# Performance work log

Hardware: AMD Instinct MI355X
Metric: run time of the kernel (lower is better)

## Reference

```python
import jax, jax.numpy as jnp
import numpy as np

DIM = 768
NUM_HEADS = 12
HEAD_DIM = DIM // NUM_HEADS
B, QLEN, KVLEN = 8, 512, 4096


def setup_inputs() -> dict:
    key = jax.random.key(0)
    ks = jax.random.split(key, 12)
    s = 1.0 / np.sqrt(DIM)
    return {
        "query": jax.random.normal(ks[0], (B, QLEN, DIM), jnp.float32),
        "key": jax.random.normal(ks[1], (B, KVLEN, DIM), jnp.float32),
        "value": jax.random.normal(ks[2], (B, KVLEN, DIM), jnp.float32),
        "attention_mask": jax.random.randint(ks[3], (B, QLEN, KVLEN), 0, 2, jnp.int32),
        "Wq": jax.random.normal(ks[4], (DIM, DIM), jnp.float32) * s,
        "bq": jnp.zeros((DIM,), jnp.float32),
        "Wk": jax.random.normal(ks[5], (DIM, DIM), jnp.float32) * s,
        "bk": jnp.zeros((DIM,), jnp.float32),
        "Wv": jax.random.normal(ks[6], (DIM, DIM), jnp.float32) * s,
        "bv": jnp.zeros((DIM,), jnp.float32),
        "Wo": jax.random.normal(ks[7], (DIM, DIM), jnp.float32) * s,
        "bo": jnp.zeros((DIM,), jnp.float32),
        "ln_g": jnp.ones((DIM,), jnp.float32),
        "ln_b": jnp.zeros((DIM,), jnp.float32),
    }


def _layer_norm(x, g, b, eps=1e-5):
    mu = jnp.mean(x, axis=-1, keepdims=True)
    var = jnp.var(x, axis=-1, keepdims=True)
    return (x - mu) * jax.lax.rsqrt(var + eps) * g + b


def reference(query, key, value, attention_mask, Wq, bq, Wk, bk, Wv, bv, Wo, bo, ln_g, ln_b):
    # LayerNorm on query only (as in original), then QKV projections
    q = _layer_norm(query, ln_g, ln_b)
    q = q @ Wq.T + bq                      # [B, Q, D]
    k = key @ Wk.T + bk                    # [B, KV, D]
    v = value @ Wv.T + bv                  # [B, KV, D]

    # split heads: [B, H, S, Dh]
    q = q.reshape(B, QLEN, NUM_HEADS, HEAD_DIM).transpose(0, 2, 1, 3)
    k = k.reshape(B, KVLEN, NUM_HEADS, HEAD_DIM).transpose(0, 2, 1, 3)
    v = v.reshape(B, KVLEN, NUM_HEADS, HEAD_DIM).transpose(0, 2, 1, 3)

    scale = HEAD_DIM ** -0.5
    scores = jnp.einsum("bhqd,bhkd->bhqk", q, k) * scale  # [B, H, Q, KV]
    mask = (attention_mask == 1)[:, None, :, :]            # broadcast over heads
    scores = jnp.where(mask, -jnp.inf, scores)
    attn = jax.nn.softmax(scores, axis=-1)
    # dropout layers are identity in eval mode
    out = jnp.einsum("bhqk,bhkd->bhqd", attn, v)           # [B, H, Q, Dh]
    out = out.transpose(0, 2, 1, 3).reshape(B, QLEN, DIM)
    out = out @ Wo.T + bo
    return out
```

## Files before the change

### kernel.cpp

```cpp
#include <hip/hip_runtime.h>
#include <hip/hip_bf16.h>

typedef __bf16 bf16;
typedef bf16 bf16x8 __attribute__((ext_vector_type(8)));
typedef bf16 bf16x4 __attribute__((ext_vector_type(4)));
typedef short s16x4 __attribute__((ext_vector_type(4)));
typedef float f32x4 __attribute__((ext_vector_type(4)));

#define NB 8
#define QLEN 512
#define KVL 4096
#define DIM 768
#define NH 12
#define HD 64

#if __has_builtin(__builtin_amdgcn_mfma_f32_16x16x16_bf16)
static __device__ __forceinline__ f32x4 pv16(bf16x4 a, bf16x4 b, f32x4 c) {
  return __builtin_amdgcn_mfma_f32_16x16x16_bf16(a, b, c, 0, 0, 0);
}
#else
static __device__ __forceinline__ f32x4 pv16(bf16x4 a, bf16x4 b, f32x4 c) {
  return __builtin_amdgcn_mfma_f32_16x16x16bf16_1k(
      __builtin_bit_cast(s16x4, a), __builtin_bit_cast(s16x4, b), c, 0, 0, 0);
}
#endif

__global__ __launch_bounds__(256) void ln_q(const float* __restrict__ x,
    const float* __restrict__ g, const float* __restrict__ beta,
    bf16* __restrict__ out)
{
  int row  = blockIdx.x * 4 + (threadIdx.x >> 6);
  int lane = threadIdx.x & 63;
  const float* rp = x + (size_t)row * DIM;
  f32x4 v[3];
  float s = 0.f, s2 = 0.f;
#pragma unroll
  for (int i = 0; i < 3; ++i) {
    v[i] = *reinterpret_cast<const f32x4*>(rp + (i * 64 + lane) * 4);
#pragma unroll
    for (int j = 0; j < 4; ++j) { s += v[i][j]; s2 += v[i][j] * v[i][j]; }
  }
#pragma unroll
  for (int o = 1; o < 64; o <<= 1) { s += __shfl_xor(s, o); s2 += __shfl_xor(s2, o); }
  float mean = s * (1.f / 768.f);
  float var  = s2 * (1.f / 768.f) - mean * mean;
  float rstd = rsqrtf(var + 1e-5f);
#pragma unroll
  for (int i = 0; i < 3; ++i) {
    int c = (i * 64 + lane) * 4;
    f32x4 gg = *reinterpret_cast<const f32x4*>(g + c);
    f32x4 bb = *reinterpret_cast<const f32x4*>(beta + c);
    bf16x4 o4;
#pragma unroll
    for (int j = 0; j < 4; ++j) o4[j] = (bf16)((v[i][j] - mean) * rstd * gg[j] + bb[j]);
    *reinterpret_cast<bf16x4*>(out + (size_t)row * DIM + c) = o4;
  }
}

__global__ __launch_bounds__(256) void pack_mask(const int* __restrict__ m,
                                                 unsigned* __restrict__ bits)
{
  const int total = NB * QLEN * KVL;
  int stride = gridDim.x * blockDim.x;
  for (int i = blockIdx.x * blockDim.x + threadIdx.x; i < total; i += stride) {
    unsigned long long bal = __ballot(m[i] == 1);
    int lane = threadIdx.x & 63;
    if ((lane & 31) == 0)
      bits[i >> 5] = (unsigned)(bal >> (lane & 32));
  }
}

__global__ __launch_bounds__(256) void conv_w(
    const float* __restrict__ w0, const float* __restrict__ w1,
    const float* __restrict__ w2, const float* __restrict__ w3,
    bf16* __restrict__ o0, bf16* __restrict__ o1,
    bf16* __restrict__ o2, bf16* __restrict__ o3)
{
  int sel = blockIdx.y;
  const float* s = sel == 0 ? w0 : sel == 1 ? w1 : sel == 2 ? w2 : w3;
  bf16* d = sel == 0 ? o0 : sel == 1 ? o1 : sel == 2 ? o2 : o3;
  int i = (blockIdx.x * 256 + threadIdx.x) * 8;
  f32x4 a = *reinterpret_cast<const f32x4*>(s + i);
  f32x4 b = *reinterpret_cast<const f32x4*>(s + i + 4);
  bf16x8 v;
#pragma unroll
  for (int j = 0; j < 4; ++j) { v[j] = (bf16)a[j]; v[4 + j] = (bf16)b[j]; }
  *reinterpret_cast<bf16x8*>(d + i) = v;
}

template<bool A_IS_BF16, bool OUT_BF16>
__global__ __launch_bounds__(256) void gemm128(const void* __restrict__ Aptr,
    const bf16* __restrict__ W, const float* __restrict__ bias,
    void* __restrict__ Out)
{
  const int K = 768, N = 768;
  __shared__ __align__(16) bf16 a_s[128][72];
  __shared__ __align__(16) bf16 b_s[128][72];
  int raw = blockIdx.x;
  int nt = (raw >> 3) % 6;
  int mt = ((raw >> 3) / 6) * 8 + (raw & 7);
  int m0 = mt * 128, n0 = nt * 128;
  int tid = threadIdx.x;
  int lane = tid & 63, wid = tid >> 6;
  int l16 = lane & 15, g4 = lane >> 4;
  int wm = wid >> 1, wn = wid & 1;
  f32x4 acc[4][4] = {};

  for (int k0 = 0; k0 < K; k0 += 64) {
#pragma unroll
    for (int i = 0; i < 4; ++i) {
      int oct = tid + i * 256;
      int row = oct >> 3, col = (oct & 7) * 8;
      bf16x8 av;
      if constexpr (A_IS_BF16) {
        av = *reinterpret_cast<const bf16x8*>((const bf16*)Aptr + (size_t)(m0 + row) * K + k0 + col);
      } else {
        const float* ap = (const float*)Aptr + (size_t)(m0 + row) * K + k0 + col;
        f32x4 f0 = *reinterpret_cast<const f32x4*>(ap);
        f32x4 f1 = *reinterpret_cast<const f32x4*>(ap + 4);
#pragma unroll
        for (int j = 0; j < 4; ++j) { av[j] = (bf16)f0[j]; av[4 + j] = (bf16)f1[j]; }
      }
      *reinterpret_cast<bf16x8*>(&a_s[row][col]) = av;

      *reinterpret_cast<bf16x8*>(&b_s[row][col]) =
          *reinterpret_cast<const bf16x8*>(W + (size_t)(n0 + row) * K + k0 + col);
    }
    __syncthreads();
#pragma unroll
    for (int kk = 0; kk < 2; ++kk) {
      bf16x8 af[4], bfv[4];
#pragma unroll
      for (int mi = 0; mi < 4; ++mi)
        af[mi] = *reinterpret_cast<const bf16x8*>(&a_s[wm * 64 + mi * 16 + l16][kk * 32 + g4 * 8]);
#pragma unroll
      for (int ni = 0; ni < 4; ++ni)
        bfv[ni] = *reinterpret_cast<const bf16x8*>(&b_s[wn * 64 + ni * 16 + l16][kk * 32 + g4 * 8]);
#pragma unroll
      for (int mi = 0; mi < 4; ++mi)
#pragma unroll
        for (int ni = 0; ni < 4; ++ni)
          acc[mi][ni] = __builtin_amdgcn_mfma_f32_16x16x32_bf16(af[mi], bfv[ni], acc[mi][ni], 0, 0, 0);
    }
    __syncthreads();
  }
#pragma unroll
  for (int mi = 0; mi < 4; ++mi)
#pragma unroll
    for (int ni = 0; ni < 4; ++ni) {
      int col = n0 + wn * 64 + ni * 16 + l16;
      float bv = bias[col];
#pragma unroll
      for (int j = 0; j < 4; ++j) {
        int row = m0 + wm * 64 + mi * 16 + g4 * 4 + j;
        float v = acc[mi][ni][j] + bv;
        if constexpr (OUT_BF16) ((bf16*)Out)[(size_t)row * N + col] = (bf16)v;
        else                    ((float*)Out)[(size_t)row * N + col] = v;
      }
    }
}

__global__ __launch_bounds__(256, 4) void attn(const bf16* __restrict__ Qp,
    const bf16* __restrict__ Kp, const bf16* __restrict__ Vp,
    const unsigned* __restrict__ mbits, bf16* __restrict__ Ctx)
{
  int h = blockIdx.x, qt = blockIdx.y, b = blockIdx.z;
  int tid = threadIdx.x, lane = tid & 63, wid = tid >> 6;
  int g4 = lane >> 4, l16 = lane & 15;
  __shared__ __align__(16) bf16 k_s[2][64][72];
  __shared__ __align__(16) bf16 v_s[2][64][72];

  int qrow_w = b * QLEN + qt * 64 + wid * 16;
  int q = qrow_w + l16;

  bf16x8 qf[2];
#pragma unroll
  for (int kk = 0; kk < 2; ++kk) {
    bf16x8 t = *reinterpret_cast<const bf16x8*>(Qp + (size_t)q * DIM + h * HD + kk * 32 + g4 * 8);
#pragma unroll
    for (int j = 0; j < 8; ++j) qf[kk][j] = (bf16)((float)t[j] * 0.125f);
  }

  const bf16* Kb = Kp + (size_t)b * KVL * DIM + h * HD;
  const bf16* Vb = Vp + (size_t)b * KVL * DIM + h * HD;
  const unsigned* mrow = mbits + (size_t)q * (KVL / 32);

  f32x4 oacc[4] = {};
  float m_r = -1e30f, l_r = 0.f;

  int krow = tid >> 3, kcol = (tid & 7) * 8;
  int vkv = tid & 31, vd0 = (tid >> 5) * 8;

  bf16x8 kreg0, kreg1, vreg0, vreg1;
  unsigned m0w, m1w, m0n, m1n;

  kreg0 = *reinterpret_cast<const bf16x8*>(Kb + (size_t)krow * DIM + kcol);
  kreg1 = *reinterpret_cast<const bf16x8*>(Kb + (size_t)(krow + 32) * DIM + kcol);
  vreg0 = *reinterpret_cast<const bf16x8*>(Vb + (size_t)vkv * DIM + vd0);
  vreg1 = *reinterpret_cast<const bf16x8*>(Vb + (size_t)(vkv + 32) * DIM + vd0);
  m0w = mrow[0]; m1w = mrow[1];
  *reinterpret_cast<bf16x8*>(&k_s[0][krow][kcol]) = kreg0;
  *reinterpret_cast<bf16x8*>(&k_s[0][krow + 32][kcol]) = kreg1;
#pragma unroll
  for (int j = 0; j < 8; ++j) {
    v_s[0][vd0 + j][vkv] = vreg0[j];
    v_s[0][vd0 + j][vkv + 32] = vreg1[j];
  }
  __syncthreads();

  const int NT = KVL / 64;
  for (int t = 0; t < NT; ++t) {
    int buf = t & 1;
    if (t + 1 < NT) {
      int kv0n = (t + 1) * 64;
      kreg0 = *reinterpret_cast<const bf16x8*>(Kb + (size_t)(kv0n + krow) * DIM + kcol);
      kreg1 = *reinterpret_cast<const bf16x8*>(Kb + (size_t)(kv0n + krow + 32) * DIM + kcol);
      vreg0 = *reinterpret_cast<const bf16x8*>(Vb + (size_t)(kv0n + vkv) * DIM + vd0);
      vreg1 = *reinterpret_cast<const bf16x8*>(Vb + (size_t)(kv0n + vkv + 32) * DIM + vd0);
      m0n = mrow[(t + 1) * 2];
      m1n = mrow[(t + 1) * 2 + 1];
    }

    f32x4 sacc[4] = {};
#pragma unroll
    for (int nb = 0; nb < 4; ++nb)
#pragma unroll
      for (int kk = 0; kk < 2; ++kk) {
        bf16x8 kf = *reinterpret_cast<const bf16x8*>(&k_s[buf][nb * 16 + l16][kk * 32 + g4 * 8]);
        sacc[nb] = __builtin_amdgcn_mfma_f32_16x16x32_bf16(kf, qf[kk], sacc[nb], 0, 0, 0);
      }

    float sv[16];
#pragma unroll
    for (int nb = 0; nb < 4; ++nb) {
      unsigned w = (nb < 2) ? m0w : m1w;
#pragma unroll
      for (int r = 0; r < 4; ++r) {
        int bit = (nb & 1) * 16 + g4 * 4 + r;
        sv[nb * 4 + r] = ((w >> bit) & 1u) ? -1e30f : sacc[nb][r];
      }
    }

    float a0 = fmaxf(fmaxf(sv[0], sv[1]), sv[2]);
    float a1 = fmaxf(fmaxf(sv[3], sv[4]), sv[5]);
    float a2 = fmaxf(fmaxf(sv[6], sv[7]), sv[8]);
    float a3 = fmaxf(fmaxf(sv[9], sv[10]), sv[11]);
    float a4 = fmaxf(fmaxf(sv[12], sv[13]), sv[14]);
    float b0 = fmaxf(fmaxf(a0, a1), sv[15]);
    float b1 = fmaxf(fmaxf(a2, a3), a4);
    float tm = fmaxf(b0, b1);
    tm = fmaxf(tm, __shfl_xor(tm, 16));
    tm = fmaxf(tm, __shfl_xor(tm, 32));

    if (!__all(tm <= m_r)) {
      float mnew = fmaxf(m_r, tm);
      float corr = __expf(m_r - mnew);
      m_r = mnew;
      l_r *= corr;
#pragma unroll
      for (int db = 0; db < 4; ++db)
#pragma unroll
        for (int r = 0; r < 4; ++r) oacc[db][r] *= corr;
    }
    float p[16];
#pragma unroll
    for (int i = 0; i < 16; ++i) p[i] = __expf(sv[i] - m_r);
    float sm[8];
#pragma unroll
    for (int i = 0; i < 8; ++i) sm[i] = p[i] + p[i + 8];
#pragma unroll
    for (int i = 0; i < 4; ++i) sm[i] += sm[i + 4];
    float ts = (sm[0] + sm[1]) + (sm[2] + sm[3]);
    ts += __shfl_xor(ts, 16);
    ts += __shfl_xor(ts, 32);
    l_r += ts;

    bf16x4 pq[4];
#pragma unroll
    for (int nb = 0; nb < 4; ++nb)
#pragma unroll
      for (int j = 0; j < 4; ++j) pq[nb][j] = (bf16)p[nb * 4 + j];

#pragma unroll
    for (int db = 0; db < 4; ++db)
#pragma unroll
      for (int nb = 0; nb < 4; ++nb) {
        bf16x4 vf = *reinterpret_cast<const bf16x4*>(&v_s[buf][db * 16 + l16][nb * 16 + g4 * 4]);
        oacc[db] = pv16(vf, pq[nb], oacc[db]);
      }

    if (t + 1 < NT) {
      int nb2 = buf ^ 1;
      *reinterpret_cast<bf16x8*>(&k_s[nb2][krow][kcol]) = kreg0;
      *reinterpret_cast<bf16x8*>(&k_s[nb2][krow + 32][kcol]) = kreg1;
#pragma unroll
      for (int j = 0; j < 8; ++j) {
        v_s[nb2][vd0 + j][vkv] = vreg0[j];
        v_s[nb2][vd0 + j][vkv + 32] = vreg1[j];
      }
      m0w = m0n; m1w = m1n;
    }
    __syncthreads();
  }

  bf16* o_base = &k_s[0][0][0] + (size_t)wid * 16 * 72;
  float inv = 1.f / l_r;
#pragma unroll
  for (int db = 0; db < 4; ++db) {
    bf16x4 t4;
#pragma unroll
    for (int r = 0; r < 4; ++r) t4[r] = (bf16)(oacc[db][r] * inv);
    *reinterpret_cast<bf16x4*>(o_base + l16 * 72 + db * 16 + g4 * 4) = t4;
  }
#pragma unroll
  for (int pass = 0; pass < 2; ++pass) {
    int row = (lane >> 3) + pass * 8;
    int c8 = (lane & 7) * 8;
    bf16x8 v = *reinterpret_cast<const bf16x8*>(o_base + row * 72 + c8);
    *reinterpret_cast<bf16x8*>(Ctx + (size_t)(qrow_w + row) * DIM + h * HD + c8) = v;
  }
}

extern "C" void kernel_launch(void* const* d_in, const int* in_sizes, int n_in,
                              void* d_out, int out_size, void* d_ws, size_t ws_size,
                              hipStream_t stream) {
  const float* query = (const float*)d_in[0];
  const float* key   = (const float*)d_in[1];
  const float* value = (const float*)d_in[2];
  const int*   amask = (const int*)d_in[3];
  const float* Wq = (const float*)d_in[4];
  const float* bq = (const float*)d_in[5];
  const float* Wk = (const float*)d_in[6];
  const float* bk = (const float*)d_in[7];
  const float* Wv = (const float*)d_in[8];
  const float* bv = (const float*)d_in[9];
  const float* Wo = (const float*)d_in[10];
  const float* bo = (const float*)d_in[11];
  const float* ln_g = (const float*)d_in[12];
  const float* ln_b = (const float*)d_in[13];

  char* ws = (char*)d_ws;
  bf16* qln = (bf16*)ws;      ws += (size_t)NB * QLEN * DIM * 2;
  bf16* Qp  = (bf16*)ws;      ws += (size_t)NB * QLEN * DIM * 2;
  bf16* Kp  = (bf16*)ws;      ws += (size_t)NB * KVL * DIM * 2;
  bf16* Vp  = (bf16*)ws;      ws += (size_t)NB * KVL * DIM * 2;
  bf16* Ctx = (bf16*)ws;      ws += (size_t)NB * QLEN * DIM * 2;
  unsigned* mbits = (unsigned*)ws; ws += (size_t)NB * QLEN * (KVL / 32) * 4;
  bf16* Wqb = (bf16*)ws;      ws += (size_t)DIM * DIM * 2;
  bf16* Wkb = (bf16*)ws;      ws += (size_t)DIM * DIM * 2;
  bf16* Wvb = (bf16*)ws;      ws += (size_t)DIM * DIM * 2;
  bf16* Wob = (bf16*)ws;

  ln_q<<<NB * QLEN / 4, 256, 0, stream>>>(query, ln_g, ln_b, qln);
  pack_mask<<<1024, 256, 0, stream>>>(amask, mbits);
  conv_w<<<dim3(DIM * DIM / (256 * 8), 4), 256, 0, stream>>>(Wq, Wk, Wv, Wo, Wqb, Wkb, Wvb, Wob);

  gemm128<true,  true><<<(NB * QLEN / 128) * 6, 256, 0, stream>>>(qln,   Wqb, bq, Qp);
  gemm128<false, true><<<(NB * KVL  / 128) * 6, 256, 0, stream>>>(key,   Wkb, bk, Kp);
  gemm128<false, true><<<(NB * KVL  / 128) * 6, 256, 0, stream>>>(value, Wvb, bv, Vp);

  attn<<<dim3(NH, QLEN / 64, NB), 256, 0, stream>>>(Qp, Kp, Vp, mbits, Ctx);

  gemm128<true, false><<<(NB * QLEN / 128) * 6, 256, 0, stream>>>(Ctx, Wob, bo, (float*)d_out);
}
```

Measured before the change: 359.1 us.

## Split KV range across two wave groups per attention block with merge

Result: slower. 366.8 us (+2.1%).

```diff
diff --git a/kernel.cpp b/kernel.cpp
--- a/kernel.cpp
+++ b/kernel.cpp
@@ -160,17 +160,20 @@
     }
 }
 
-__global__ __launch_bounds__(256, 4) void attn(const bf16* __restrict__ Qp,
+__global__ __launch_bounds__(512, 6) void attn(const bf16* __restrict__ Qp,
     const bf16* __restrict__ Kp, const bf16* __restrict__ Vp,
     const unsigned* __restrict__ mbits, bf16* __restrict__ Ctx)
 {
   int h = blockIdx.x, qt = blockIdx.y, b = blockIdx.z;
-  int tid = threadIdx.x, lane = tid & 63, wid = tid >> 6;
+  int tid = threadIdx.x;
+  int grp = tid >> 8;
+  int tg  = tid & 255;
+  int lane = tid & 63, wid4 = (tid >> 6) & 3;
   int g4 = lane >> 4, l16 = lane & 15;
   __shared__ __align__(16) bf16 k_s[2][64][72];
   __shared__ __align__(16) bf16 v_s[2][64][72];
 
-  int qrow_w = b * QLEN + qt * 64 + wid * 16;
+  int qrow_w = b * QLEN + qt * 64 + wid4 * 16;
   int q = qrow_w + l16;
 
   bf16x8 qf[2];
@@ -181,59 +184,49 @@
     for (int j = 0; j < 8; ++j) qf[kk][j] = (bf16)((float)t[j] * 0.125f);
   }
 
-  const bf16* Kb = Kp + (size_t)b * KVL * DIM + h * HD;
-  const bf16* Vb = Vp + (size_t)b * KVL * DIM + h * HD;
-  const unsigned* mrow = mbits + (size_t)q * (KVL / 32);
+  int kv_base = grp * (KVL / 2);
+  const bf16* Kb = Kp + ((size_t)b * KVL + kv_base) * DIM + h * HD;
+  const bf16* Vb = Vp + ((size_t)b * KVL + kv_base) * DIM + h * HD;
+  const unsigned* mrow = mbits + (size_t)q * (KVL / 32) + (kv_base >> 5);
 
   f32x4 oacc[4] = {};
   float m_r = -1e30f, l_r = 0.f;
 
-  int krow = tid >> 3, kcol = (tid & 7) * 8;
-  int vkv = tid & 31, vd0 = (tid >> 5) * 8;
-
-  bf16x8 kreg0, kreg1, vreg0, vreg1;
-  unsigned m0w, m1w, m0n, m1n;
-
-  kreg0 = *reinterpret_cast<const bf16x8*>(Kb + (size_t)krow * DIM + kcol);
-  kreg1 = *reinterpret_cast<const bf16x8*>(Kb + (size_t)(krow + 32) * DIM + kcol);
-  vreg0 = *reinterpret_cast<const bf16x8*>(Vb + (size_t)vkv * DIM + vd0);
-  vreg1 = *reinterpret_cast<const bf16x8*>(Vb + (size_t)(vkv + 32) * DIM + vd0);
-  m0w = mrow[0]; m1w = mrow[1];
-  *reinterpret_cast<bf16x8*>(&k_s[0][krow][kcol]) = kreg0;
-  *reinterpret_cast<bf16x8*>(&k_s[0][krow + 32][kcol]) = kreg1;
-#pragma unroll
-  for (int j = 0; j < 8; ++j) {
-    v_s[0][vd0 + j][vkv] = vreg0[j];
-    v_s[0][vd0 + j][vkv + 32] = vreg1[j];
-  }
-  __syncthreads();
-
-  const int NT = KVL / 64;
-  for (int t = 0; t < NT; ++t) {
-    int buf = t & 1;
-    if (t + 1 < NT) {
-      int kv0n = (t + 1) * 64;
-      kreg0 = *reinterpret_cast<const bf16x8*>(Kb + (size_t)(kv0n + krow) * DIM + kcol);
-      kreg1 = *reinterpret_cast<const bf16x8*>(Kb + (size_t)(kv0n + krow + 32) * DIM + kcol);
-      vreg0 = *reinterpret_cast<const bf16x8*>(Vb + (size_t)(kv0n + vkv) * DIM + vd0);
-      vreg1 = *reinterpret_cast<const bf16x8*>(Vb + (size_t)(kv0n + vkv + 32) * DIM + vd0);
-      m0n = mrow[(t + 1) * 2];
-      m1n = mrow[(t + 1) * 2 + 1];
-    }
+  for (int kv0 = 0; kv0 < KVL / 2; kv0 += 64) {
+    {
+      int row = tg >> 3, col = (tg & 7) * 8;
+      *reinterpret_cast<bf16x8*>(&k_s[grp][row][col]) =
+          *reinterpret_cast<const bf16x8*>(Kb + (size_t)(kv0 + row) * DIM + col);
+      *reinterpret_cast<bf16x8*>(&k_s[grp][row + 32][col]) =
+          *reinterpret_cast<const bf16x8*>(Kb + (size_t)(kv0 + row + 32) * DIM + col);
+    }
+    {
+      int kv = tg & 31, d0 = (tg >> 5) * 8;
+      bf16x8 va = *reinterpret_cast<const bf16x8*>(Vb + (size_t)(kv0 + kv) * DIM + d0);
+      bf16x8 vb2 = *reinterpret_cast<const bf16x8*>(Vb + (size_t)(kv0 + kv + 32) * DIM + d0);
+#pragma unroll
+      for (int j = 0; j < 8; ++j) {
+        v_s[grp][d0 + j][kv] = va[j];
+        v_s[grp][d0 + j][kv + 32] = vb2[j];
+      }
+    }
+    __syncthreads();
 
     f32x4 sacc[4] = {};
 #pragma unroll
     for (int nb = 0; nb < 4; ++nb)
 #pragma unroll
       for (int kk = 0; kk < 2; ++kk) {
-        bf16x8 kf = *reinterpret_cast<const bf16x8*>(&k_s[buf][nb * 16 + l16][kk * 32 + g4 * 8]);
+        bf16x8 kf = *reinterpret_cast<const bf16x8*>(&k_s[grp][nb * 16 + l16][kk * 32 + g4 * 8]);
         sacc[nb] = __builtin_amdgcn_mfma_f32_16x16x32_bf16(kf, qf[kk], sacc[nb], 0, 0, 0);
       }
 
+    unsigned w0 = mrow[kv0 >> 5];
+    unsigned w1 = mrow[(kv0 >> 5) + 1];
     float sv[16];
 #pragma unroll
     for (int nb = 0; nb < 4; ++nb) {
-      unsigned w = (nb < 2) ? m0w : m1w;
+      unsigned w = (nb < 2) ? w0 : w1;
 #pragma unroll
       for (int r = 0; r < 4; ++r) {
         int bit = (nb & 1) * 16 + g4 * 4 + r;
@@ -285,25 +278,38 @@
     for (int db = 0; db < 4; ++db)
 #pragma unroll
       for (int nb = 0; nb < 4; ++nb) {
-        bf16x4 vf = *reinterpret_cast<const bf16x4*>(&v_s[buf][db * 16 + l16][nb * 16 + g4 * 4]);
+        bf16x4 vf = *reinterpret_cast<const bf16x4*>(&v_s[grp][db * 16 + l16][nb * 16 + g4 * 4]);
         oacc[db] = pv16(vf, pq[nb], oacc[db]);
       }
-
-    if (t + 1 < NT) {
-      int nb2 = buf ^ 1;
-      *reinterpret_cast<bf16x8*>(&k_s[nb2][krow][kcol]) = kreg0;
-      *reinterpret_cast<bf16x8*>(&k_s[nb2][krow + 32][kcol]) = kreg1;
-#pragma unroll
-      for (int j = 0; j < 8; ++j) {
-        v_s[nb2][vd0 + j][vkv] = vreg0[j];
-        v_s[nb2][vd0 + j][vkv + 32] = vreg1[j];
-      }
-      m0w = m0n; m1w = m1n;
-    }
     __syncthreads();
   }
 
-  bf16* o_base = &k_s[0][0][0] + (size_t)wid * 16 * 72;
+  float* mbuf = reinterpret_cast<float*>(&k_s[0][0][0]);
+  if (grp == 1) {
+    float* pp = mbuf + ((size_t)wid4 * 64 + lane) * 18;
+#pragma unroll
+    for (int db = 0; db < 4; ++db)
+#pragma unroll
+      for (int r = 0; r < 4; ++r) pp[db * 4 + r] = oacc[db][r];
+    pp[16] = m_r;
+    pp[17] = l_r;
+  }
+  __syncthreads();
+  if (grp == 1) return;
+
+  {
+    const float* pp = mbuf + ((size_t)wid4 * 64 + lane) * 18;
+    float m2 = pp[16], l2 = pp[17];
+    float ms = fmaxf(m_r, m2);
+    float e1 = __expf(m_r - ms), e2 = __expf(m2 - ms);
+    l_r = l_r * e1 + l2 * e2;
+#pragma unroll
+    for (int db = 0; db < 4; ++db)
+#pragma unroll
+      for (int r = 0; r < 4; ++r) oacc[db][r] = oacc[db][r] * e1 + pp[db * 4 + r] * e2;
+  }
+
+  bf16* o_base = &v_s[0][0][0] + (size_t)wid4 * 16 * 72;
   float inv = 1.f / l_r;
 #pragma unroll
   for (int db = 0; db < 4; ++db) {
@@ -359,7 +365,7 @@
   gemm128<false, true><<<(NB * KVL  / 128) * 6, 256, 0, stream>>>(key,   Wkb, bk, Kp);
   gemm128<false, true><<<(NB * KVL  / 128) * 6, 256, 0, stream>>>(value, Wvb, bv, Vp);
 
-  attn<<<dim3(NH, QLEN / 64, NB), 256, 0, stream>>>(Qp, Kp, Vp, mbits, Ctx);
+  attn<<<dim3(NH, QLEN / 64, NB), 512, 0, stream>>>(Qp, Kp, Vp, mbits, Ctx);
 
   gemm128<true, false><<<(NB * QLEN / 128) * 6, 256, 0, stream>>>(Ctx, Wob, bo, (float*)d_out);
 }
```

## Load K fragments directly from global into registers, bypassing shared memory

Applied to the files above, without the earlier changes.

Result: slower. 475.8 us (+32.5%).

```diff
diff --git a/kernel.cpp b/kernel.cpp
--- a/kernel.cpp
+++ b/kernel.cpp
@@ -160,14 +160,13 @@
     }
 }
 
-__global__ __launch_bounds__(256, 4) void attn(const bf16* __restrict__ Qp,
+__global__ __launch_bounds__(256, 3) void attn(const bf16* __restrict__ Qp,
     const bf16* __restrict__ Kp, const bf16* __restrict__ Vp,
     const unsigned* __restrict__ mbits, bf16* __restrict__ Ctx)
 {
   int h = blockIdx.x, qt = blockIdx.y, b = blockIdx.z;
   int tid = threadIdx.x, lane = tid & 63, wid = tid >> 6;
   int g4 = lane >> 4, l16 = lane & 15;
-  __shared__ __align__(16) bf16 k_s[2][64][72];
   __shared__ __align__(16) bf16 v_s[2][64][72];
 
   int qrow_w = b * QLEN + qt * 64 + wid * 16;
@@ -182,25 +181,28 @@
   }
 
   const bf16* Kb = Kp + (size_t)b * KVL * DIM + h * HD;
+  const bf16* Klane = Kb + (size_t)l16 * DIM + g4 * 8;
   const bf16* Vb = Vp + (size_t)b * KVL * DIM + h * HD;
   const unsigned* mrow = mbits + (size_t)q * (KVL / 32);
 
   f32x4 oacc[4] = {};
   float m_r = -1e30f, l_r = 0.f;
 
-  int krow = tid >> 3, kcol = (tid & 7) * 8;
   int vkv = tid & 31, vd0 = (tid >> 5) * 8;
 
-  bf16x8 kreg0, kreg1, vreg0, vreg1;
+  bf16x8 vreg0, vreg1;
   unsigned m0w, m1w, m0n, m1n;
-
-  kreg0 = *reinterpret_cast<const bf16x8*>(Kb + (size_t)krow * DIM + kcol);
-  kreg1 = *reinterpret_cast<const bf16x8*>(Kb + (size_t)(krow + 32) * DIM + kcol);
+  bf16x8 kfA[8], kfB[8];
+
+#pragma unroll
+  for (int nb = 0; nb < 4; ++nb)
+#pragma unroll
+    for (int kk = 0; kk < 2; ++kk)
+      kfA[nb * 2 + kk] = *reinterpret_cast<const bf16x8*>(
+          Klane + (size_t)(nb * 16) * DIM + kk * 32);
   vreg0 = *reinterpret_cast<const bf16x8*>(Vb + (size_t)vkv * DIM + vd0);
   vreg1 = *reinterpret_cast<const bf16x8*>(Vb + (size_t)(vkv + 32) * DIM + vd0);
   m0w = mrow[0]; m1w = mrow[1];
-  *reinterpret_cast<bf16x8*>(&k_s[0][krow][kcol]) = kreg0;
-  *reinterpret_cast<bf16x8*>(&k_s[0][krow + 32][kcol]) = kreg1;
 #pragma unroll
   for (int j = 0; j < 8; ++j) {
     v_s[0][vd0 + j][vkv] = vreg0[j];
@@ -209,12 +211,17 @@
   __syncthreads();
 
   const int NT = KVL / 64;
-  for (int t = 0; t < NT; ++t) {
+  auto body = [&](int t, bf16x8 (&kfc)[8], bf16x8 (&kfn)[8]) {
     int buf = t & 1;
     if (t + 1 < NT) {
       int kv0n = (t + 1) * 64;
-      kreg0 = *reinterpret_cast<const bf16x8*>(Kb + (size_t)(kv0n + krow) * DIM + kcol);
-      kreg1 = *reinterpret_cast<const bf16x8*>(Kb + (size_t)(kv0n + krow + 32) * DIM + kcol);
+      const bf16* Kl = Klane + (size_t)kv0n * DIM;
+#pragma unroll
+      for (int nb = 0; nb < 4; ++nb)
+#pragma unroll
+        for (int kk = 0; kk < 2; ++kk)
+          kfn[nb * 2 + kk] = *reinterpret_cast<const bf16x8*>(
+              Kl + (size_t)(nb * 16) * DIM + kk * 32);
       vreg0 = *reinterpret_cast<const bf16x8*>(Vb + (size_t)(kv0n + vkv) * DIM + vd0);
       vreg1 = *reinterpret_cast<const bf16x8*>(Vb + (size_t)(kv0n + vkv + 32) * DIM + vd0);
       m0n = mrow[(t + 1) * 2];
@@ -225,10 +232,8 @@
 #pragma unroll
     for (int nb = 0; nb < 4; ++nb)
 #pragma unroll
-      for (int kk = 0; kk < 2; ++kk) {
-        bf16x8 kf = *reinterpret_cast<const bf16x8*>(&k_s[buf][nb * 16 + l16][kk * 32 + g4 * 8]);
-        sacc[nb] = __builtin_amdgcn_mfma_f32_16x16x32_bf16(kf, qf[kk], sacc[nb], 0, 0, 0);
-      }
+      for (int kk = 0; kk < 2; ++kk)
+        sacc[nb] = __builtin_amdgcn_mfma_f32_16x16x32_bf16(kfc[nb * 2 + kk], qf[kk], sacc[nb], 0, 0, 0);
 
     float sv[16];
 #pragma unroll
@@ -291,8 +296,6 @@
 
     if (t + 1 < NT) {
       int nb2 = buf ^ 1;
-      *reinterpret_cast<bf16x8*>(&k_s[nb2][krow][kcol]) = kreg0;
-      *reinterpret_cast<bf16x8*>(&k_s[nb2][krow + 32][kcol]) = kreg1;
 #pragma unroll
       for (int j = 0; j < 8; ++j) {
         v_s[nb2][vd0 + j][vkv] = vreg0[j];
@@ -301,9 +304,14 @@
       m0w = m0n; m1w = m1n;
     }
     __syncthreads();
-  }
-
-  bf16* o_base = &k_s[0][0][0] + (size_t)wid * 16 * 72;
+  };
+
+  for (int tt = 0; tt < NT / 2; ++tt) {
+    body(2 * tt,     kfA, kfB);
+    body(2 * tt + 1, kfB, kfA);
+  }
+
+  bf16* o_base = &v_s[0][0][0] + (size_t)wid * 16 * 72;
   float inv = 1.f / l_r;
 #pragma unroll
   for (int db = 0; db < 4; ++db) {
```
